# Optimization experiments

Measured on AMD Instinct MI355X. Metric: run time of the kernel, lower is better.

## Reference

```python
import jax, jax.numpy as jnp
import numpy as np

N_EMBD = 1024
N_HEAD = 16
HEAD_DIM = N_EMBD // N_HEAD
B, T = 8, 1024


def setup_inputs() -> dict:
    key = jax.random.key(0)
    k1, k2, k3, k4 = jax.random.split(key, 4)
    x = jax.random.normal(k1, (B, T, N_EMBD), dtype=jnp.float32)
    # nn.Linear weight shapes: qkv (3C, C) no bias; proj (C, C) with bias
    w_qkv = jax.random.normal(k2, (3 * N_EMBD, N_EMBD), dtype=jnp.float32) * 0.02
    w_proj = jax.random.normal(k3, (N_EMBD, N_EMBD), dtype=jnp.float32) * 0.02
    b_proj = jax.random.normal(k4, (N_EMBD,), dtype=jnp.float32) * 0.02
    return {"x": x, "w_qkv": w_qkv, "w_proj": w_proj, "b_proj": b_proj}


def reference(x, w_qkv, w_proj, b_proj):
    Bq, Tq, C = x.shape
    qkv = jnp.einsum('btc,dc->btd', x, w_qkv)  # (B,T,3C)
    q, k, v = jnp.split(qkv, 3, axis=-1)
    def heads(t):
        return t.reshape(Bq, Tq, N_HEAD, HEAD_DIM).transpose(0, 2, 1, 3)  # (B,H,T,D)
    q, k, v = heads(q), heads(k), heads(v)
    scale = 1.0 / np.sqrt(HEAD_DIM).astype(np.float32)
    att = jnp.einsum('bhqd,bhkd->bhqk', q, k) * scale  # (B,H,T,T)
    causal = jnp.tril(jnp.ones((Tq, Tq), dtype=bool))
    att = jnp.where(causal, att, -jnp.inf)
    att = jax.nn.softmax(att, axis=-1)
    # dropout: eval mode -> identity
    y = jnp.einsum('bhqk,bhkd->bhqd', att, v)
    y = y.transpose(0, 2, 1, 3).reshape(Bq, Tq, C)
    return jnp.einsum('btc,dc->btd', y, w_proj) + b_proj
```

## Files before the change

kernel.cpp:

```cpp
#include <hip/hip_runtime.h>
#include <stdint.h>


#define Bn 8
#define Tn 1024
#define Cn 1024
#define Hn 16
#define Dn 64
#define Mn (Bn * Tn)
#define NQKV (3 * Cn)
#define QKS 2048

typedef unsigned short u16;
typedef float f32x4 __attribute__((ext_vector_type(4)));
typedef __bf16 bf16x8 __attribute__((ext_vector_type(8)));
typedef unsigned short ushx8 __attribute__((ext_vector_type(8)));
typedef unsigned short ushx4 __attribute__((ext_vector_type(4)));

__device__ __forceinline__ u16 f2bf(float f) {
  unsigned int u = __float_as_uint(f);
  u += 0x7fffu + ((u >> 16) & 1u);
  return (u16)(u >> 16);
}
__device__ __forceinline__ u16 f2bf_rna(float f) {
  return (u16)((__float_as_uint(f) + 0x8000u) >> 16);
}

__device__ __forceinline__ f32x4 mfma_bf16(ushx8 a, ushx8 b, f32x4 c) {
  return __builtin_amdgcn_mfma_f32_16x16x32_bf16(
      __builtin_bit_cast(bf16x8, a), __builtin_bit_cast(bf16x8, b), c, 0, 0, 0);
}

__device__ __forceinline__ void async16(const u16* g, u16* l) {
  __builtin_amdgcn_global_load_lds(
      (__attribute__((address_space(1))) void*)(void*)g,
      (__attribute__((address_space(3))) void*)l, 16, 0, 0);
}

template <int CTRL>
__device__ __forceinline__ float dppmov(float v) {
  return __builtin_bit_cast(float, __builtin_amdgcn_update_dpp(
      0, __builtin_bit_cast(int, v), CTRL, 0xf, 0xf, true));
}
__device__ __forceinline__ float red16max(float v) {
  v = fmaxf(v, dppmov<0xB1>(v));
  v = fmaxf(v, dppmov<0x4E>(v));
  v = fmaxf(v, dppmov<0x141>(v));
  v = fmaxf(v, dppmov<0x140>(v));
  return v;
}
__device__ __forceinline__ float red16sum(float v) {
  v += dppmov<0xB1>(v);
  v += dppmov<0x4E>(v);
  v += dppmov<0x141>(v);
  v += dppmov<0x140>(v);
  return v;
}

__global__ void cast3_kernel(const float* __restrict__ a, u16* __restrict__ oa, int na4,
                             const float* __restrict__ b, u16* __restrict__ ob, int nb4,
                             const float* __restrict__ c, u16* __restrict__ oc, int nc4) {
  int i = blockIdx.x * blockDim.x + threadIdx.x;
  const float* in;
  u16* out;
  if (i < na4) { in = a; out = oa; }
  else if (i < na4 + nb4) { in = b; out = ob; i -= na4; }
  else if (i < na4 + nb4 + nc4) { in = c; out = oc; i -= na4 + nb4; }
  else return;
  float4 v = ((const float4*)in)[i];
  ushx4 o = { f2bf(v.x), f2bf(v.y), f2bf(v.z), f2bf(v.w) };
  ((ushx4*)out)[i] = o;
}

#define SLOG2E 0.18033688011112042f
template <int QKV>
__global__ __launch_bounds__(256, 4) void gemm_bt(
    const u16* __restrict__ A, const u16* __restrict__ Bw,
    void* __restrict__ Cout, u16* __restrict__ vt,
    const float* __restrict__ bias, int N, int K) {
  __shared__ alignas(16) u16 As[128 * 32];
  __shared__ alignas(16) u16 Bs[128 * 32];

  const int tid = threadIdx.x;
  const int lane = tid & 63;
  const int wv = tid >> 6;
  const int quad = lane >> 4;
  const int l16 = lane & 15;
  const int m0 = blockIdx.x * 128;
  const int n0 = blockIdx.y * 128;
  const int wm = (wv >> 1) * 64;
  const int wn = (wv & 1) * 64;

  f32x4 acc[4][4];
#pragma unroll
  for (int i = 0; i < 4; ++i)
#pragma unroll
    for (int j = 0; j < 4; ++j) acc[i][j] = (f32x4){0.f, 0.f, 0.f, 0.f};

  const int r0 = tid >> 2;
  const int cc0 = tid & 3;
  const int gkc0 = cc0 ^ ((r0 >> 1) & 3);
  const int r1 = r0 + 64;
  const int gkc1 = cc0 ^ ((r1 >> 1) & 3);
  const u16* gA0 = A + (size_t)(m0 + r0) * K + gkc0 * 8;
  const u16* gA1 = A + (size_t)(m0 + r1) * K + gkc1 * 8;
  const u16* gB0 = Bw + (size_t)(n0 + r0) * K + gkc0 * 8;
  const u16* gB1 = Bw + (size_t)(n0 + r1) * K + gkc1 * 8;
  u16* lA0 = As + tid * 8;
  u16* lA1 = As + (256 + tid) * 8;
  u16* lB0 = Bs + tid * 8;
  u16* lB1 = Bs + (256 + tid) * 8;

  const u16* pa[4];
  const u16* pb[4];
#pragma unroll
  for (int mi = 0; mi < 4; ++mi) {
    int ra = wm + mi * 16 + l16;
    pa[mi] = As + ra * 32 + (quad ^ ((ra >> 1) & 3)) * 8;
    int rb = wn + mi * 16 + l16;
    pb[mi] = Bs + rb * 32 + (quad ^ ((rb >> 1) & 3)) * 8;
  }

  for (int k0 = 0; k0 < K; k0 += 32) {
    async16(gA0 + k0, lA0);
    async16(gA1 + k0, lA1);
    async16(gB0 + k0, lB0);
    async16(gB1 + k0, lB1);
    __syncthreads();
    ushx8 af[4], bf[4];
#pragma unroll
    for (int i = 0; i < 4; ++i) {
      af[i] = *(const ushx8*)pa[i];
      bf[i] = *(const ushx8*)pb[i];
    }
#pragma unroll
    for (int mi = 0; mi < 4; ++mi)
#pragma unroll
      for (int ni = 0; ni < 4; ++ni)
        acc[mi][ni] = mfma_bf16(af[mi], bf[ni], acc[mi][ni]);
    __syncthreads();
  }

  if constexpr (QKV) {
    if (n0 < 2 * Cn) {
      const float sc = (n0 < Cn) ? SLOG2E : 1.f;
#pragma unroll
      for (int mi = 0; mi < 4; ++mi) {
#pragma unroll
        for (int ni = 0; ni < 4; ++ni) {
          int col = n0 + wn + ni * 16 + l16;
#pragma unroll
          for (int i = 0; i < 4; ++i) {
            int row = m0 + wm + mi * 16 + quad * 4 + i;
            ((u16*)Cout)[(size_t)row * QKS + col] = f2bf(acc[mi][ni][i] * sc);
          }
        }
      }
    } else {
#pragma unroll
      for (int mi = 0; mi < 4; ++mi) {
#pragma unroll
        for (int ni = 0; ni < 4; ++ni) {
          int colV = n0 + wn + ni * 16 + l16 - 2 * Cn;
          int hh = colV >> 6, dd = colV & 63;
          int row0 = m0 + wm + mi * 16 + quad * 4;
          int bb = row0 >> 10, tt = row0 & 1023;
          unsigned int lo = (unsigned int)f2bf(acc[mi][ni][0]) |
                            ((unsigned int)f2bf(acc[mi][ni][1]) << 16);
          unsigned int hi = (unsigned int)f2bf(acc[mi][ni][2]) |
                            ((unsigned int)f2bf(acc[mi][ni][3]) << 16);
          uint2 pk = {lo, hi};
          *(uint2*)&vt[((size_t)(bb * Hn + hh) * Dn + dd) * Tn + tt] = pk;
        }
      }
    }
  } else {
#pragma unroll
    for (int mi = 0; mi < 4; ++mi) {
#pragma unroll
      for (int ni = 0; ni < 4; ++ni) {
        int col = n0 + wn + ni * 16 + l16;
        float bv = bias[col];
#pragma unroll
        for (int i = 0; i < 4; ++i) {
          int row = m0 + wm + mi * 16 + quad * 4 + i;
          ((float*)Cout)[(size_t)row * N + col] = acc[mi][ni][i] + bv;
        }
      }
    }
  }
}

__global__ __launch_bounds__(512, 4) void attn_kernel(
    const u16* __restrict__ qk, const u16* __restrict__ vt,
    u16* __restrict__ out) {
  const int j = blockIdx.x, h = blockIdx.y, b = blockIdx.z;
  const int tid = threadIdx.x;
  const int lane = tid & 63;
  const int wv = tid >> 6;
  const int quad = lane >> 4;
  const int l16 = lane & 15;

  __shared__ alignas(16) u16 Ks[2][64 * 64];
  __shared__ alignas(16) u16 Vts[2][64 * 64];
  __shared__ alignas(16) u16 Ps[8][16 * 72];

  const u16* qb = qk + (size_t)b * Tn * QKS + h * Dn;
  const u16* kb = qk + (size_t)b * Tn * QKS + Cn + h * Dn;
  const u16* vtb = vt + (size_t)(b * Hn + h) * Dn * Tn;

  const int srow = tid >> 3;
  const int scc = tid & 7;
  const int sgc = scc ^ (srow & 7);
  u16* pswv = Ps[wv];

#pragma unroll 1
  for (int ph = 0; ph < 2; ++ph) {
    const int qt = ph ? (7 - j) : j;
    const int q0w = qt * 128 + wv * 16;
    const int ntiles = 2 * qt + 2;
    const int tdiag = q0w >> 6;

    ushx8 qf[2];
    {
      const u16* qp = qb + (size_t)(q0w + l16) * QKS + quad * 8;
      qf[0] = *(const ushx8*)qp;
      qf[1] = *(const ushx8*)(qp + 32);
    }

    f32x4 o[4];
#pragma unroll
    for (int nt = 0; nt < 4; ++nt) o[nt] = (f32x4){0.f, 0.f, 0.f, 0.f};
    float mrow[4], lrow[4];
#pragma unroll
    for (int i = 0; i < 4; ++i) { mrow[i] = -__builtin_inff(); lrow[i] = 0.f; }

    __syncthreads();

    async16(kb + (size_t)srow * QKS + sgc * 8, Ks[0] + tid * 8);
    async16(vtb + (size_t)srow * Tn + sgc * 8, Vts[0] + tid * 8);

#pragma unroll 1
    for (int t = 0; t < ntiles; ++t) {
      const int kv0 = t * 64;
      const int bi = t & 1;
      __syncthreads();

      if (t + 1 < ntiles) {
        const int nkv0 = kv0 + 64;
        async16(kb + (size_t)(nkv0 + srow) * QKS + sgc * 8, Ks[bi ^ 1] + tid * 8);
        async16(vtb + (size_t)srow * Tn + nkv0 + sgc * 8, Vts[bi ^ 1] + tid * 8);
      }

      if (t > tdiag) continue;

      const u16* ks = Ks[bi];
      const u16* vs = Vts[bi];
      f32x4 s[4];
#pragma unroll
      for (int nt = 0; nt < 4; ++nt) s[nt] = (f32x4){0.f, 0.f, 0.f, 0.f};
#pragma unroll
      for (int nt = 0; nt < 4; ++nt) {
        const int rb = nt * 16 + l16;
        ushx8 b0 = *(const ushx8*)(ks + rb * 64 + (quad ^ (rb & 7)) * 8);
        ushx8 b1 = *(const ushx8*)(ks + rb * 64 + ((quad + 4) ^ (rb & 7)) * 8);
        s[nt] = mfma_bf16(qf[0], b0, s[nt]);
        s[nt] = mfma_bf16(qf[1], b1, s[nt]);
      }

      if (t == tdiag) {
#pragma unroll
        for (int i = 0; i < 4; ++i) {
          const int qr = q0w + quad * 4 + i;
          float vv[4];
          float rmax = -__builtin_inff();
#pragma unroll
          for (int nt = 0; nt < 4; ++nt) {
            float v = s[nt][i];
            if ((kv0 + nt * 16 + l16) > qr) v = -__builtin_inff();
            vv[nt] = v;
            rmax = fmaxf(rmax, v);
          }
          rmax = red16max(rmax);
          const float mnew = fmaxf(mrow[i], rmax);
          const float al = __builtin_amdgcn_exp2f(mrow[i] - mnew);
          mrow[i] = mnew;
          float rsum = 0.f;
#pragma unroll
          for (int nt = 0; nt < 4; ++nt) {
            float p = __builtin_amdgcn_exp2f(vv[nt] - mnew);
            rsum += p;
            pswv[(quad * 4 + i) * 72 + nt * 16 + l16] = f2bf_rna(p);
          }
          lrow[i] = lrow[i] * al + rsum;
#pragma unroll
          for (int nt = 0; nt < 4; ++nt) o[nt][i] *= al;
        }
      } else {
#pragma unroll
        for (int i = 0; i < 4; ++i) {
          float rmax = fmaxf(fmaxf(s[0][i], s[1][i]), fmaxf(s[2][i], s[3][i]));
          rmax = red16max(rmax);
          const float mnew = fmaxf(mrow[i], rmax);
          const float al = __builtin_amdgcn_exp2f(mrow[i] - mnew);
          mrow[i] = mnew;
          float rsum = 0.f;
#pragma unroll
          for (int nt = 0; nt < 4; ++nt) {
            float p = __builtin_amdgcn_exp2f(s[nt][i] - mnew);
            rsum += p;
            pswv[(quad * 4 + i) * 72 + nt * 16 + l16] = f2bf_rna(p);
          }
          lrow[i] = lrow[i] * al + rsum;
#pragma unroll
          for (int nt = 0; nt < 4; ++nt) o[nt][i] *= al;
        }
      }

      ushx8 pf0, pf1;
      {
        const u16* pp = pswv + l16 * 72 + quad * 8;
        pf0 = *(const ushx8*)pp;
        pf1 = *(const ushx8*)(pp + 32);
      }

#pragma unroll
      for (int nt = 0; nt < 4; ++nt) {
        const int rb = nt * 16 + l16;
        ushx8 v0 = *(const ushx8*)(vs + rb * 64 + (quad ^ (rb & 7)) * 8);
        ushx8 v1 = *(const ushx8*)(vs + rb * 64 + ((quad + 4) ^ (rb & 7)) * 8);
        o[nt] = mfma_bf16(pf0, v0, o[nt]);
        o[nt] = mfma_bf16(pf1, v1, o[nt]);
      }
    }

#pragma unroll
    for (int i = 0; i < 4; ++i) {
      const float inv = 1.f / red16sum(lrow[i]);
      const int trow = q0w + quad * 4 + i;
      u16* op = out + ((size_t)(b * Tn + trow)) * Cn + h * Dn + l16;
#pragma unroll
      for (int nt = 0; nt < 4; ++nt) op[nt * 16] = f2bf(o[nt][i] * inv);
    }
  }
}

extern "C" void kernel_launch(void* const* d_in, const int* in_sizes, int n_in,
                              void* d_out, int out_size, void* d_ws, size_t ws_size,
                              hipStream_t stream) {
  const float* x = (const float*)d_in[0];
  const float* w_qkv = (const float*)d_in[1];
  const float* w_proj = (const float*)d_in[2];
  const float* b_proj = (const float*)d_in[3];
  float* out = (float*)d_out;
  char* ws = (char*)d_ws;

  u16* xb     = (u16*)(ws);
  u16* wqkvb  = (u16*)(ws + 16777216);
  u16* wprojb = (u16*)(ws + 23068672);
  u16* qkb    = (u16*)(ws + 25165824);
  u16* vtb    = (u16*)(ws + 58720256);
  u16* yb     = (u16*)(ws + 75497472);

  cast3_kernel<<<12288, 256, 0, stream>>>(x, xb, 2097152,
                                          w_qkv, wqkvb, 786432,
                                          w_proj, wprojb, 262144);

  gemm_bt<1><<<dim3(Mn / 128, NQKV / 128), 256, 0, stream>>>(
      xb, wqkvb, (void*)qkb, vtb, nullptr, NQKV, Cn);

  attn_kernel<<<dim3(4, Hn, Bn), 512, 0, stream>>>(qkb, vtb, yb);

  gemm_bt<0><<<dim3(Mn / 128, Cn / 128), 256, 0, stream>>>(
      yb, wprojb, (void*)out, nullptr, b_proj, Cn, Cn);
}
```

Baseline: 226.5 us.

## Replace QKV GEMM with 256x256-tile, 8-wave pipelined async-load kernel

Result: slower. 238.0 us (+5.1%).

```diff
diff --git a/kernel.cpp b/kernel.cpp
--- a/kernel.cpp
+++ b/kernel.cpp
@@ -10,6 +10,8 @@
 #define Mn (Bn * Tn)
 #define NQKV (3 * Cn)
 #define QKS 2048
+#define NTILE 16
+#define GQKV_BLOCKS 384
 
 typedef unsigned short u16;
 typedef float f32x4 __attribute__((ext_vector_type(4)));
@@ -73,6 +75,144 @@
 }
 
 #define SLOG2E 0.18033688011112042f
+
+__global__ __launch_bounds__(512, 2) void gemm256_qkv(
+    const u16* __restrict__ A, const u16* __restrict__ Bw,
+    u16* __restrict__ qk, u16* __restrict__ vt) {
+  __shared__ alignas(16) u16 lds[65536];
+
+  const int tid = threadIdx.x;
+  const int lane = tid & 63;
+  const int wv = tid >> 6;
+  const int quad = lane >> 4;
+  const int l16 = lane & 15;
+  const int wr = wv >> 2;
+  const int wc = wv & 3;
+
+  const int z = (blockIdx.x & 7) * (GQKV_BLOCKS / 8) + (blockIdx.x >> 3);
+  const int m0 = (z & 31) * 256;
+  const int n0 = (z >> 5) * 256;
+
+  const u16* gA = A + (size_t)m0 * Cn;
+  const u16* gB = Bw + (size_t)n0 * Cn;
+
+  const int r0s = tid >> 2;
+  const int q0s = (tid & 3) ^ ((r0s >> 1) & 3);
+  const int c1s = 512 + tid;
+  const int r1s = c1s >> 2;
+  const int q1s = (c1s & 3) ^ ((r1s >> 1) & 3);
+  const int so0 = r0s * Cn + q0s * 8;
+  const int so1 = r1s * Cn + q1s * 8;
+
+  auto stage = [&](int region, int buf, int kk, const u16* gbase, int kt) {
+    u16* dst = lds + region + (buf * 2 + kk) * 8192 + tid * 8;
+    const u16* src = gbase + kt * 64 + kk * 32;
+    async16(src + so0, dst);
+    async16(src + so1, dst + 4096);
+  };
+
+  const int sread = (quad ^ ((l16 >> 1) & 3)) * 8;
+  const int aoff = (wr * 128 + l16) * 32 + sread;
+  const int boff = 32768 + (wc * 64 + l16) * 32 + sread;
+
+  f32x4 acc[8][4];
+#pragma unroll
+  for (int i = 0; i < 8; ++i)
+#pragma unroll
+    for (int j = 0; j < 4; ++j) acc[i][j] = (f32x4){0.f, 0.f, 0.f, 0.f};
+  ushx8 af[4], bfr[4];
+
+  stage(0, 0, 0, gA, 0);      stage(32768, 0, 0, gB, 0);
+  stage(0, 0, 1, gA, 0);      stage(32768, 0, 1, gB, 0);
+  stage(0, 1, 0, gA, 1);      stage(32768, 1, 0, gB, 1);
+  asm volatile("s_waitcnt vmcnt(4)" ::: "memory");
+  __builtin_amdgcn_s_barrier();
+  asm volatile("" ::: "memory");
+
+#define PH(buf, kk, mg, LOADB, DOVM, ...)                                      \
+  {                                                                            \
+    const u16* hb_ = lds + ((buf) * 2 + (kk)) * 8192;                          \
+    const u16* ab_ = hb_ + aoff + (mg) * 2048;                                 \
+    af[0] = *(const ushx8*)(ab_);                                              \
+    af[1] = *(const ushx8*)(ab_ + 512);                                        \
+    af[2] = *(const ushx8*)(ab_ + 1024);                                       \
+    af[3] = *(const ushx8*)(ab_ + 1536);                                       \
+    if (LOADB) {                                                               \
+      const u16* bb_ = hb_ + boff;                                             \
+      bfr[0] = *(const ushx8*)(bb_);                                           \
+      bfr[1] = *(const ushx8*)(bb_ + 512);                                     \
+      bfr[2] = *(const ushx8*)(bb_ + 1024);                                    \
+      bfr[3] = *(const ushx8*)(bb_ + 1536);                                    \
+    }                                                                          \
+    __VA_ARGS__;                                                               \
+    asm volatile("" ::: "memory");                                             \
+    __builtin_amdgcn_s_barrier();                                              \
+    asm volatile("s_waitcnt lgkmcnt(0)" ::: "memory");                         \
+    __builtin_amdgcn_s_setprio(1);                                             \
+    _Pragma("unroll") for (int mi_ = 0; mi_ < 4; ++mi_) {                      \
+      _Pragma("unroll") for (int ni_ = 0; ni_ < 4; ++ni_) {                    \
+        acc[(mg) * 4 + mi_][ni_] =                                             \
+            mfma_bf16(af[mi_], bfr[ni_], acc[(mg) * 4 + mi_][ni_]);            \
+      }                                                                        \
+    }                                                                          \
+    __builtin_amdgcn_s_setprio(0);                                             \
+    if (DOVM) asm volatile("s_waitcnt vmcnt(4)" ::: "memory");                 \
+    asm volatile("" ::: "memory");                                             \
+    __builtin_amdgcn_s_barrier();                                              \
+    asm volatile("" ::: "memory");                                             \
+  }
+
+#pragma unroll 1
+  for (int it = 0; it < 8; ++it) {
+    const int t = it * 2;
+    const int ktp1 = t + 1;
+    const int kt2 = (t + 2 < NTILE) ? t + 2 : NTILE - 1;
+    const int kt3 = (t + 3 < NTILE) ? t + 3 : NTILE - 1;
+    PH(0, 0, 0, 1, 0, stage(0, 1, 1, gA, ktp1); stage(32768, 1, 1, gB, ktp1))
+    PH(0, 0, 1, 0, 0, )
+    PH(0, 1, 0, 1, 0, stage(0, 0, 0, gA, kt2))
+    PH(0, 1, 1, 0, 1, stage(32768, 0, 0, gB, kt2))
+    PH(1, 0, 0, 1, 0, stage(0, 0, 1, gA, kt2); stage(32768, 0, 1, gB, kt2))
+    PH(1, 0, 1, 0, 0, )
+    PH(1, 1, 0, 1, 0, stage(0, 1, 0, gA, kt3))
+    PH(1, 1, 1, 0, 1, stage(32768, 1, 0, gB, kt3))
+  }
+#undef PH
+  asm volatile("s_waitcnt vmcnt(0)" ::: "memory");
+
+  if (n0 < 2 * Cn) {
+    const float sc = (n0 < Cn) ? SLOG2E : 1.f;
+#pragma unroll
+    for (int mi = 0; mi < 8; ++mi) {
+#pragma unroll
+      for (int ni = 0; ni < 4; ++ni) {
+        const int col = n0 + wc * 64 + ni * 16 + l16;
+        const int row = m0 + wr * 128 + mi * 16 + quad * 4;
+#pragma unroll
+        for (int i = 0; i < 4; ++i)
+          qk[(size_t)(row + i) * QKS + col] = f2bf(acc[mi][ni][i] * sc);
+      }
+    }
+  } else {
+#pragma unroll
+    for (int mi = 0; mi < 8; ++mi) {
+#pragma unroll
+      for (int ni = 0; ni < 4; ++ni) {
+        const int colV = n0 - 2 * Cn + wc * 64 + ni * 16 + l16;
+        const int hh = colV >> 6, dd = colV & 63;
+        const int row0 = m0 + wr * 128 + mi * 16 + quad * 4;
+        const int bb = row0 >> 10, tt = row0 & 1023;
+        unsigned int lo = (unsigned int)f2bf(acc[mi][ni][0]) |
+                          ((unsigned int)f2bf(acc[mi][ni][1]) << 16);
+        unsigned int hi = (unsigned int)f2bf(acc[mi][ni][2]) |
+                          ((unsigned int)f2bf(acc[mi][ni][3]) << 16);
+        uint2 pk = {lo, hi};
+        *(uint2*)&vt[((size_t)(bb * Hn + hh) * Dn + dd) * Tn + tt] = pk;
+      }
+    }
+  }
+}
+
 template <int QKV>
 __global__ __launch_bounds__(256, 4) void gemm_bt(
     const u16* __restrict__ A, const u16* __restrict__ Bw,
@@ -366,8 +506,7 @@
                                           w_qkv, wqkvb, 786432,
                                           w_proj, wprojb, 262144);
 
-  gemm_bt<1><<<dim3(Mn / 128, NQKV / 128), 256, 0, stream>>>(
-      xb, wqkvb, (void*)qkb, vtb, nullptr, NQKV, Cn);
+  gemm256_qkv<<<GQKV_BLOCKS, 512, 0, stream>>>(xb, wqkvb, qkb, vtb);
 
   attn_kernel<<<dim3(4, Hn, Bn), 512, 0, stream>>>(qkb, vtb, yb);
 
```

## Replace GEMMs with 4-stage pipelined 256x128 tile kernel and XCD-aware block mapping

Applied to the files above, without the earlier changes.

Result: faster. 219.8 us (-3.0%).

```diff
diff --git a/kernel.cpp b/kernel.cpp
--- a/kernel.cpp
+++ b/kernel.cpp
@@ -73,87 +73,125 @@
 }
 
 #define SLOG2E 0.18033688011112042f
-template <int QKV>
-__global__ __launch_bounds__(256, 4) void gemm_bt(
+
+template <int MODE>
+__global__ __launch_bounds__(512, 2) void gemm_8ph(
     const u16* __restrict__ A, const u16* __restrict__ Bw,
     void* __restrict__ Cout, u16* __restrict__ vt,
-    const float* __restrict__ bias, int N, int K) {
-  __shared__ alignas(16) u16 As[128 * 32];
-  __shared__ alignas(16) u16 Bs[128 * 32];
+    const float* __restrict__ bias) {
+  __shared__ alignas(16) u16 lds[49152];
 
   const int tid = threadIdx.x;
   const int lane = tid & 63;
   const int wv = tid >> 6;
   const int quad = lane >> 4;
   const int l16 = lane & 15;
-  const int m0 = blockIdx.x * 128;
-  const int n0 = blockIdx.y * 128;
-  const int wm = (wv >> 1) * 64;
-  const int wn = (wv & 1) * 64;
+  const int wr = wv >> 1;
+  const int wc = wv & 1;
+
+  const int xcd = blockIdx.x & 7;
+  const int loc = blockIdx.x >> 3;
+  const int m0 = (xcd * 4 + (loc & 3)) * 256;
+  const int n0 = (loc >> 2) * 128;
+
+  const u16* gA = A + (size_t)m0 * Cn;
+  const u16* gB = Bw + (size_t)n0 * Cn;
+
+  const int r0s = tid >> 2;
+  const int q0s = (tid & 3) ^ ((r0s >> 1) & 3);
+  const int c1s = 512 + tid;
+  const int r1s = c1s >> 2;
+  const int q1s = (c1s & 3) ^ ((r1s >> 1) & 3);
+  const int so0 = r0s * Cn + q0s * 8;
+  const int so1 = r1s * Cn + q1s * 8;
+
+  auto stageA = [&](int slot, int h) {
+    u16* dst = lds + slot * 8192 + tid * 8;
+    const u16* src = gA + (h >> 1) * 64 + (h & 1) * 32;
+    async16(src + so0, dst);
+    async16(src + so1, dst + 4096);
+  };
+  auto stageB = [&](int slot, int h) {
+    u16* dst = lds + 32768 + slot * 4096 + tid * 8;
+    const u16* src = gB + (h >> 1) * 64 + (h & 1) * 32;
+    async16(src + so0, dst);
+  };
+
+  const int sread = (quad ^ ((l16 >> 1) & 3)) * 8;
+  const int aoff = (wr * 64 + l16) * 32 + sread;
+  const int boff = 32768 + (wc * 64 + l16) * 32 + sread;
 
   f32x4 acc[4][4];
 #pragma unroll
   for (int i = 0; i < 4; ++i)
 #pragma unroll
     for (int j = 0; j < 4; ++j) acc[i][j] = (f32x4){0.f, 0.f, 0.f, 0.f};
-
-  const int r0 = tid >> 2;
-  const int cc0 = tid & 3;
-  const int gkc0 = cc0 ^ ((r0 >> 1) & 3);
-  const int r1 = r0 + 64;
-  const int gkc1 = cc0 ^ ((r1 >> 1) & 3);
-  const u16* gA0 = A + (size_t)(m0 + r0) * K + gkc0 * 8;
-  const u16* gA1 = A + (size_t)(m0 + r1) * K + gkc1 * 8;
-  const u16* gB0 = Bw + (size_t)(n0 + r0) * K + gkc0 * 8;
-  const u16* gB1 = Bw + (size_t)(n0 + r1) * K + gkc1 * 8;
-  u16* lA0 = As + tid * 8;
-  u16* lA1 = As + (256 + tid) * 8;
-  u16* lB0 = Bs + tid * 8;
-  u16* lB1 = Bs + (256 + tid) * 8;
-
-  const u16* pa[4];
-  const u16* pb[4];
-#pragma unroll
-  for (int mi = 0; mi < 4; ++mi) {
-    int ra = wm + mi * 16 + l16;
-    pa[mi] = As + ra * 32 + (quad ^ ((ra >> 1) & 3)) * 8;
-    int rb = wn + mi * 16 + l16;
-    pb[mi] = Bs + rb * 32 + (quad ^ ((rb >> 1) & 3)) * 8;
+  ushx8 af[4], bfr[4];
+
+  stageA(0, 0); stageB(0, 0);
+  stageA(1, 1); stageB(1, 1);
+  stageA(2, 2); stageB(2, 2);
+  asm volatile("s_waitcnt vmcnt(6)" ::: "memory");
+  __builtin_amdgcn_s_barrier();
+  asm volatile("" ::: "memory");
+
+#define PH(slot, sslot, hd)                                                    \
+  {                                                                            \
+    const u16* ab_ = lds + (slot) * 8192 + aoff;                               \
+    af[0] = *(const ushx8*)(ab_);                                              \
+    af[1] = *(const ushx8*)(ab_ + 512);                                        \
+    af[2] = *(const ushx8*)(ab_ + 1024);                                       \
+    af[3] = *(const ushx8*)(ab_ + 1536);                                       \
+    const u16* bb_ = lds + (slot) * 4096 + boff;                               \
+    bfr[0] = *(const ushx8*)(bb_);                                             \
+    bfr[1] = *(const ushx8*)(bb_ + 512);                                       \
+    bfr[2] = *(const ushx8*)(bb_ + 1024);                                      \
+    bfr[3] = *(const ushx8*)(bb_ + 1536);                                      \
+    stageA((sslot), (hd));                                                     \
+    stageB((sslot), (hd));                                                     \
+    asm volatile("" ::: "memory");                                             \
+    __builtin_amdgcn_s_barrier();                                              \
+    asm volatile("s_waitcnt lgkmcnt(0)" ::: "memory");                         \
+    __builtin_amdgcn_s_setprio(1);                                             \
+    _Pragma("unroll") for (int mi_ = 0; mi_ < 4; ++mi_) {                      \
+      _Pragma("unroll") for (int ni_ = 0; ni_ < 4; ++ni_) {                    \
+        acc[mi_][ni_] = mfma_bf16(af[mi_], bfr[ni_], acc[mi_][ni_]);           \
+      }                                                                        \
+    }                                                                          \
+    __builtin_amdgcn_s_setprio(0);                                             \
+    asm volatile("s_waitcnt vmcnt(6)" ::: "memory");                           \
+    asm volatile("" ::: "memory");                                             \
+    __builtin_amdgcn_s_barrier();                                              \
+    asm volatile("" ::: "memory");                                             \
   }
 
-  for (int k0 = 0; k0 < K; k0 += 32) {
-    async16(gA0 + k0, lA0);
-    async16(gA1 + k0, lA1);
-    async16(gB0 + k0, lB0);
-    async16(gB1 + k0, lB1);
-    __syncthreads();
-    ushx8 af[4], bf[4];
-#pragma unroll
-    for (int i = 0; i < 4; ++i) {
-      af[i] = *(const ushx8*)pa[i];
-      bf[i] = *(const ushx8*)pb[i];
-    }
-#pragma unroll
-    for (int mi = 0; mi < 4; ++mi)
-#pragma unroll
-      for (int ni = 0; ni < 4; ++ni)
-        acc[mi][ni] = mfma_bf16(af[mi], bf[ni], acc[mi][ni]);
-    __syncthreads();
+#pragma unroll 1
+  for (int it = 0; it < 8; ++it) {
+    const int p = it * 4;
+    const int h0 = (p + 3 < 32) ? p + 3 : 31;
+    const int h1 = (p + 4 < 32) ? p + 4 : 31;
+    const int h2 = (p + 5 < 32) ? p + 5 : 31;
+    const int h3 = (p + 6 < 32) ? p + 6 : 31;
+    PH(0, 3, h0)
+    PH(1, 0, h1)
+    PH(2, 1, h2)
+    PH(3, 2, h3)
   }
-
-  if constexpr (QKV) {
+#undef PH
+  asm volatile("s_waitcnt vmcnt(0)" ::: "memory");
+
+  if constexpr (MODE) {
     if (n0 < 2 * Cn) {
       const float sc = (n0 < Cn) ? SLOG2E : 1.f;
 #pragma unroll
       for (int mi = 0; mi < 4; ++mi) {
 #pragma unroll
         for (int ni = 0; ni < 4; ++ni) {
-          int col = n0 + wn + ni * 16 + l16;
-#pragma unroll
-          for (int i = 0; i < 4; ++i) {
-            int row = m0 + wm + mi * 16 + quad * 4 + i;
-            ((u16*)Cout)[(size_t)row * QKS + col] = f2bf(acc[mi][ni][i] * sc);
-          }
+          const int col = n0 + wc * 64 + ni * 16 + l16;
+          const int row = m0 + wr * 64 + mi * 16 + quad * 4;
+#pragma unroll
+          for (int i = 0; i < 4; ++i)
+            ((u16*)Cout)[(size_t)(row + i) * QKS + col] = f2bf(acc[mi][ni][i] * sc);
         }
       }
     } else {
@@ -161,10 +199,10 @@
       for (int mi = 0; mi < 4; ++mi) {
 #pragma unroll
         for (int ni = 0; ni < 4; ++ni) {
-          int colV = n0 + wn + ni * 16 + l16 - 2 * Cn;
-          int hh = colV >> 6, dd = colV & 63;
-          int row0 = m0 + wm + mi * 16 + quad * 4;
-          int bb = row0 >> 10, tt = row0 & 1023;
+          const int colV = n0 - 2 * Cn + wc * 64 + ni * 16 + l16;
+          const int hh = colV >> 6, dd = colV & 63;
+          const int row0 = m0 + wr * 64 + mi * 16 + quad * 4;
+          const int bb = row0 >> 10, tt = row0 & 1023;
           unsigned int lo = (unsigned int)f2bf(acc[mi][ni][0]) |
                             ((unsigned int)f2bf(acc[mi][ni][1]) << 16);
           unsigned int hi = (unsigned int)f2bf(acc[mi][ni][2]) |
@@ -179,13 +217,12 @@
     for (int mi = 0; mi < 4; ++mi) {
 #pragma unroll
       for (int ni = 0; ni < 4; ++ni) {
-        int col = n0 + wn + ni * 16 + l16;
-        float bv = bias[col];
-#pragma unroll
-        for (int i = 0; i < 4; ++i) {
-          int row = m0 + wm + mi * 16 + quad * 4 + i;
-          ((float*)Cout)[(size_t)row * N + col] = acc[mi][ni][i] + bv;
-        }
+        const int col = n0 + wc * 64 + ni * 16 + l16;
+        const float bv = bias[col];
+        const int row = m0 + wr * 64 + mi * 16 + quad * 4;
+#pragma unroll
+        for (int i = 0; i < 4; ++i)
+          ((float*)Cout)[(size_t)(row + i) * Cn + col] = acc[mi][ni][i] + bv;
       }
     }
   }
@@ -366,11 +403,9 @@
                                           w_qkv, wqkvb, 786432,
                                           w_proj, wprojb, 262144);
 
-  gemm_bt<1><<<dim3(Mn / 128, NQKV / 128), 256, 0, stream>>>(
-      xb, wqkvb, (void*)qkb, vtb, nullptr, NQKV, Cn);
+  gemm_8ph<1><<<768, 512, 0, stream>>>(xb, wqkvb, (void*)qkb, vtb, nullptr);
 
   attn_kernel<<<dim3(4, Hn, Bn), 512, 0, stream>>>(qkb, vtb, yb);
 
-  gemm_bt<0><<<dim3(Mn / 128, Cn / 128), 256, 0, stream>>>(
-      yb, wprojb, (void*)out, nullptr, b_proj, Cn, Cn);
-}
+  gemm_8ph<0><<<256, 512, 0, stream>>>(yb, wprojb, (void*)out, nullptr, b_proj);
+}
```
